# Kernel optimization log

Measured on AMD Instinct MI355X. Metric: run time of the kernel, lower is better.

Reference implementation:

```python
import jax, jax.numpy as jnp
import numpy as np
from jax import lax

K = 3
PAD = 1


def conv2d(x, w, b, pad):
    out = lax.conv_general_dilated(x, w, (1, 1), [(pad, pad), (pad, pad)],
                                   dimension_numbers=('NCHW', 'OIHW', 'NCHW'))
    return out + b[None, :, None, None]


def bilinear_sample(img, y, x):
    # img [B,C,H,W]; y,x [B,K2,H,W] float coords; zero padding outside
    H, W = img.shape[2], img.shape[3]
    y0 = jnp.floor(y)
    x0 = jnp.floor(x)
    wy = y - y0
    wx = x - x0

    def corner(yc, xc, wgt):
        valid = (yc >= 0) & (yc <= H - 1) & (xc >= 0) & (xc <= W - 1)
        yi = jnp.clip(yc, 0, H - 1).astype(jnp.int32)
        xi = jnp.clip(xc, 0, W - 1).astype(jnp.int32)
        vals = jax.vmap(lambda im, a, b_: im[:, a, b_])(img, yi, xi)  # [B,C,K2,H,W]
        return vals * (wgt * valid)[:, None]

    return (corner(y0, x0, (1 - wy) * (1 - wx)) + corner(y0, x0 + 1, (1 - wy) * wx)
            + corner(y0 + 1, x0, wy * (1 - wx)) + corner(y0 + 1, x0 + 1, wy * wx))


def dcn_v2(x, off_w, off_b, w, b):
    # ModulatedDeformConvPack: conv_offset -> (o1,o2,mask); deformable 3x3 conv, stride 1, pad 1
    B, C, H, W = x.shape
    off = conv2d(x, off_w, off_b, PAD)                      # [B,27,H,W]
    o1, o2, m = jnp.split(off, 3, axis=1)
    offset = jnp.concatenate([o1, o2], axis=1)              # [B,18,H,W]
    dy = offset[:, 0::2]                                    # [B,9,H,W]
    dx = offset[:, 1::2]
    mask = jax.nn.sigmoid(m)                                # [B,9,H,W]
    ki, kj = jnp.meshgrid(jnp.arange(K), jnp.arange(K), indexing='ij')
    ki = ki.reshape(K * K).astype(x.dtype)
    kj = kj.reshape(K * K).astype(x.dtype)
    # base sampling grid: p_y = h - pad + ki, p_x = w - pad + kj
    py = (jnp.arange(H, dtype=x.dtype)[None, :] - PAD + ki[:, None])  # [9,H]
    px = (jnp.arange(W, dtype=x.dtype)[None, :] - PAD + kj[:, None])  # [9,W]
    ys = py[None, :, :, None] + dy                           # [B,9,H,W]
    xs = px[None, :, None, :] + dx
    sampled = bilinear_sample(x, ys, xs)                     # [B,C,9,H,W]
    sampled = sampled * mask[:, None]
    out = jnp.einsum('bckhw,ock->bohw', sampled, w.reshape(w.shape[0], w.shape[1], K * K))
    return out + b[None, :, None, None]


def upsample2x(x):
    B, C, H, W = x.shape
    return jax.image.resize(x, (B, C, 2 * H, 2 * W), method='bilinear')


def forward(x, ow1, ob1, w1, b1, ow2, ob2, w2, b2, rw, rb):
    h = jax.nn.elu(dcn_v2(x, ow1, ob1, w1, b1))
    h = upsample2x(h)
    h = jax.nn.elu(dcn_v2(h, ow2, ob2, w2, b2))
    res = upsample2x(conv2d(x, rw, rb, 0))
    return h + res


def setup_inputs() -> dict:
    key = jax.random.key(0)
    ks = jax.random.split(key, 12)
    Cin, Cout = 64, 64
    B, H, W = 2, 192, 192
    f = jnp.float32
    return {
        'x': jax.random.normal(ks[0], (B, Cin, H, W), dtype=f),
        'ow1': jax.random.normal(ks[1], (27, Cin, 3, 3), dtype=f) * 0.01,
        'ob1': jax.random.normal(ks[2], (27,), dtype=f) * 0.01,
        'w1': jax.random.normal(ks[3], (Cout, Cin, 3, 3), dtype=f) * (1.0 / np.sqrt(Cin * 9)),
        'b1': jnp.zeros((Cout,), dtype=f),
        'ow2': jax.random.normal(ks[4], (27, Cout, 3, 3), dtype=f) * 0.01,
        'ob2': jax.random.normal(ks[5], (27,), dtype=f) * 0.01,
        'w2': jax.random.normal(ks[6], (Cout, Cout, 3, 3), dtype=f) * (1.0 / np.sqrt(Cout * 9)),
        'b2': jnp.zeros((Cout,), dtype=f),
        'rw': jax.random.normal(ks[7], (Cout, Cin, 1, 1), dtype=f) * (1.0 / np.sqrt(Cin)),
        'rb': jnp.zeros((Cout,), dtype=f),
    }


def reference(x, ow1, ob1, w1, b1, ow2, ob2, w2, b2, rw, rb):
    return forward(x, ow1, ob1, w1, b1, ow2, ob2, w2, b2, rw, rb)
```

## Files before the change

kernel.cpp:

```cpp
#include <hip/hip_runtime.h>
#include <math.h>

typedef unsigned short u16;
typedef __attribute__((ext_vector_type(8))) short bf16x8;
typedef __attribute__((ext_vector_type(4))) float f32x4;
typedef __attribute__((ext_vector_type(4))) unsigned u32x4;

__device__ __forceinline__ u16 f2b(float f) {
    union { float f; unsigned u; } v; v.f = f;
    unsigned r = (v.u + 0x7FFF + ((v.u >> 16) & 1)) >> 16;
    return (u16)r;
}
__device__ __forceinline__ unsigned pack2(float a, float b) {
    return (unsigned)f2b(a) | ((unsigned)f2b(b) << 16);
}
__device__ __forceinline__ void bpair(unsigned u, float& lo, float& hi) {
    union { unsigned q; float f; } a, b;
    a.q = u << 16; b.q = u & 0xFFFF0000u;
    lo = a.f; hi = b.f;
}

__global__ void prep_frag(const float* __restrict__ src, u16* __restrict__ dst,
                          int G, int KCB, int NOC, int TS) {
    int idx = blockIdx.x * 256 + threadIdx.x;
    if (idx >= KCB * G * 512) return;
    int j = idx & 7, lane = (idx >> 3) & 63, rest = idx >> 9;
    int g = rest % G, kcb = rest / G;
    int oc = g * 16 + (lane & 15);
    int c = (kcb & 1) * 32 + (lane >> 4) * 8 + j;
    int k = kcb >> 1;
    float v = (oc < NOC) ? src[((size_t)oc * 64 + c) * TS + k] : 0.f;
    dst[idx] = f2b(v);
}

template<int H, int W>
__global__ __launch_bounds__(256) void nchw2nhwc_bf16(const float* __restrict__ src,
                                                      u16* __restrict__ dst) {
    const int SEG = W / 64, HW = H * W;
    int blk = blockIdx.x;
    int b = blk / (H * SEG);
    int r = blk - b * (H * SEG);
    int h = r / SEG;
    int x0 = (r - h * SEG) * 64;
    int t = threadIdx.x;
    __shared__ float lds[64][65];
    const float* sb = src + (size_t)b * 64 * HW + (size_t)h * W + x0;
    int px = t & 63, cg = t >> 6;
#pragma unroll
    for (int i = 0; i < 16; ++i) {
        int c = cg * 16 + i;
        lds[c][px] = sb[(size_t)c * HW + px];
    }
    __syncthreads();
    u16* db = dst + ((size_t)b * HW + (size_t)h * W + x0) * 64;
    int c = t & 63, pg = t >> 6;
#pragma unroll
    for (int i = 0; i < 16; ++i) {
        int p = pg * 16 + i;
        db[(size_t)p * 64 + c] = f2b(lds[c][p]);
    }
}

__global__ __launch_bounds__(256) void upsample_nhwc_bf16(const float* __restrict__ src,
                                                          u16* __restrict__ dst) {
    const int Hh = 192, Wh = 192, H = 384, W = 384;
    int ox0 = blockIdx.x * 32;
    int oy  = blockIdx.y;
    int b   = blockIdx.z;
    int t = threadIdx.x;
    int iy  = oy >> 1;
    int oy2 = (oy & 1) ? min(iy + 1, Hh - 1) : max(iy - 1, 0);
    int ix0m1 = ox0 / 2 - 1;
    __shared__ float lds[2][64][19];
    const float* sb = src + (size_t)b * 64 * Hh * Wh;
    for (int idx = t; idx < 2 * 64 * 18; idx += 256) {
        int r2 = idx / (64 * 18);
        int rem = idx - r2 * (64 * 18);
        int c = rem / 18;
        int p = rem - c * 18;
        int gx = min(max(ix0m1 + p, 0), Wh - 1);
        int gy = r2 ? oy2 : iy;
        lds[r2][c][p] = sb[((size_t)c * Hh + gy) * Wh + gx];
    }
    __syncthreads();
    int c = t & 63, j = t >> 6;
    u16* db = dst + ((size_t)b * H * W + (size_t)oy * W + ox0) * 64;
#pragma unroll
    for (int ii = 0; ii < 8; ++ii) {
        int opx = j * 8 + ii;
        int ox = ox0 + opx;
        int ix = ox >> 1;
        int oxn = (ox & 1) ? min(ix + 1, Wh - 1) : max(ix - 1, 0);
        int il = ix - ix0m1;
        int ol = oxn - ix0m1;
        float cc = lds[0][c][il], cn = lds[0][c][ol];
        float nc = lds[1][c][il], nn = lds[1][c][ol];
        db[(size_t)opx * 64 + c] = f2b(0.5625f * cc + 0.1875f * (cn + nc) + 0.0625f * nn);
    }
}

template<int H, int W>
__global__ __launch_bounds__(256, 4) void conv_off_rA(
    const u16*  __restrict__ srcT,
    const u16*  __restrict__ wf,
    const float* __restrict__ bias,
    float* __restrict__ dst)
{
    const int HW = H * W, SEGS = W / 16;
    int t = threadIdx.x;
    int wv = t >> 6, lane = t & 63, m16 = t & 15, quad = (t >> 4) & 3;
    int seg = blockIdx.x * 4 + wv;
    int b = seg / (H * SEGS);
    int r = seg - b * (H * SEGS);
    int h = r / SEGS;
    int x0 = (r - h * SEGS) * 16;

    const u16* sb = srcT + (size_t)b * HW * 64;
    float bz0 = bias[m16];
    float bz1 = (m16 < 11) ? bias[16 + m16] : 0.f;
    f32x4 acc[2] = {{bz0,bz0,bz0,bz0},{bz1,bz1,bz1,bz1}};

#pragma unroll
    for (int k = 0; k < 9; ++k) {
        const int ki = k / 3, kj = k % 3;
        int yy = h - 1 + ki;
        int xx = x0 + m16 - 1 + kj;
        bool ok = (yy >= 0 && yy < H && xx >= 0 && xx < W);
        int yc = min(max(yy, 0), H - 1);
        int xc = min(max(xx, 0), W - 1);
        const u16* base = sb + (size_t)(yc * W + xc) * 64 + quad * 8;
#pragma unroll
        for (int cb = 0; cb < 2; ++cb) {
            u32x4 raw = *(const u32x4*)(base + cb * 32);
            union { unsigned u[4]; bf16x8 v; } A;
#pragma unroll
            for (int q = 0; q < 4; ++q) A.u[q] = ok ? raw[q] : 0u;
            const u16* wrow = wf + (size_t)((k * 2 + cb) * 2) * 512 + lane * 8;
#pragma unroll
            for (int g = 0; g < 2; ++g) {
                bf16x8 bv = *(const bf16x8*)(wrow + g * 512);
                acc[g] = __builtin_amdgcn_mfma_f32_16x16x32_bf16(A.v, bv, acc[g], 0, 0, 0);
            }
        }
    }

    int xs = x0 + quad * 4;
    float* dbase = dst + (size_t)b * 27 * HW + (size_t)h * W + xs;
    *(f32x4*)(dbase + (size_t)m16 * HW) = acc[0];
    if (m16 < 11) *(f32x4*)(dbase + (size_t)(16 + m16) * HW) = acc[1];
}

__global__ __launch_bounds__(256) void conv1x1_rA(
    const u16*  __restrict__ srcT,
    const u16*  __restrict__ wf,
    const float* __restrict__ rb,
    float* __restrict__ resT)
{
    const int H = 192, W = 192, HW = H * W, SEGS = W / 16;
    int t = threadIdx.x;
    int wv = t >> 6, lane = t & 63, m16 = t & 15, quad = (t >> 4) & 3;
    int seg = blockIdx.x * 4 + wv;
    int b = seg / (H * SEGS);
    int r = seg - b * (H * SEGS);
    int h = r / SEGS;
    int x0 = (r - h * SEGS) * 16;

    const u16* base = srcT + ((size_t)b * HW + (size_t)h * W + x0 + m16) * 64 + quad * 8;
    f32x4 acc[4];
#pragma unroll
    for (int g = 0; g < 4; ++g) { float bz = rb[g * 16 + m16]; acc[g] = {bz,bz,bz,bz}; }

#pragma unroll
    for (int cb = 0; cb < 2; ++cb) {
        bf16x8 A = *(const bf16x8*)(base + cb * 32);
        const u16* wrow = wf + (size_t)(cb * 4) * 512 + lane * 8;
#pragma unroll
        for (int g = 0; g < 4; ++g) {
            bf16x8 bv = *(const bf16x8*)(wrow + g * 512);
            acc[g] = __builtin_amdgcn_mfma_f32_16x16x32_bf16(A, bv, acc[g], 0, 0, 0);
        }
    }

    int xs = x0 + quad * 4;
    float* ob = resT + ((size_t)b * HW + (size_t)h * W) * 64;
#pragma unroll
    for (int g = 0; g < 4; ++g) {
        int oc = g * 16 + m16;
#pragma unroll
        for (int rg = 0; rg < 4; ++rg)
            ob[(size_t)(xs + rg) * 64 + oc] = acc[g][rg];
    }
}

template<int H, int W, bool ADD_RES>
__global__ __launch_bounds__(256, 4) void dcn_rA(
    const u16*  __restrict__ srcT,
    const float* __restrict__ off,
    const u16*  __restrict__ wf,
    const float* __restrict__ bias,
    const float* __restrict__ resT,
    float* __restrict__ dst)
{
    const int HW = H * W, SEGS = W / 16;
    int t = threadIdx.x;
    int wv = t >> 6, lane = t & 63, m16 = t & 15, quad = (t >> 4) & 3;
    int seg = blockIdx.x * 4 + wv;
    int b = seg / (H * SEGS);
    int r = seg - b * (H * SEGS);
    int h = r / SEGS;
    int x0 = (r - h * SEGS) * 16;

    const u16* sb = srcT + (size_t)b * HW * 64;
    const float* offp = off + (size_t)b * 27 * HW + (size_t)h * W + x0 + m16;

    float dyv[9], dxv[9], msv[9];
#pragma unroll
    for (int k = 0; k < 9; ++k) {
        dyv[k] = offp[(size_t)(2 * k) * HW];
        dxv[k] = offp[(size_t)(2 * k + 1) * HW];
        msv[k] = offp[(size_t)(18 + k) * HW];
    }

    f32x4 acc[4];
#pragma unroll
    for (int g = 0; g < 4; ++g) { float bz = bias[g * 16 + m16]; acc[g] = {bz,bz,bz,bz}; }

#pragma unroll
    for (int k = 0; k < 9; ++k) {
        const int ki = k / 3, kj = k % 3;
        float mm = 1.f / (1.f + __expf(-msv[k]));
        float yf = (float)(h - 1 + ki) + dyv[k];
        float xf = (float)(x0 + m16 - 1 + kj) + dxv[k];
        float y0f = floorf(yf), x0f = floorf(xf);
        float wy = yf - y0f, wx = xf - x0f;
        int yi = (int)y0f, xi = (int)x0f;
        float vy0 = (yi >= 0 && yi < H) ? 1.f : 0.f;
        float vy1 = (yi + 1 >= 0 && yi + 1 < H) ? 1.f : 0.f;
        float vx0 = (xi >= 0 && xi < W) ? 1.f : 0.f;
        float vx1 = (xi + 1 >= 0 && xi + 1 < W) ? 1.f : 0.f;
        float w00 = (1.f - wy) * (1.f - wx) * vy0 * vx0 * mm;
        float w01 = (1.f - wy) * wx * vy0 * vx1 * mm;
        float w10 = wy * (1.f - wx) * vy1 * vx0 * mm;
        float w11 = wy * wx * vy1 * vx1 * mm;
        int y0c = min(max(yi, 0), H - 1), y1c = min(max(yi + 1, 0), H - 1);
        int x0c = min(max(xi, 0), W - 1), x1c = min(max(xi + 1, 0), W - 1);
        const u16* p00 = sb + (size_t)(y0c * W + x0c) * 64 + quad * 8;
        const u16* p01 = sb + (size_t)(y0c * W + x1c) * 64 + quad * 8;
        const u16* p10 = sb + (size_t)(y1c * W + x0c) * 64 + quad * 8;
        const u16* p11 = sb + (size_t)(y1c * W + x1c) * 64 + quad * 8;

#pragma unroll
        for (int cb = 0; cb < 2; ++cb) {
            u32x4 r00 = *(const u32x4*)(p00 + cb * 32);
            u32x4 r01 = *(const u32x4*)(p01 + cb * 32);
            u32x4 r10 = *(const u32x4*)(p10 + cb * 32);
            u32x4 r11 = *(const u32x4*)(p11 + cb * 32);
            union { unsigned u[4]; bf16x8 v; } A;
#pragma unroll
            for (int q = 0; q < 4; ++q) {
                float a0, a1, b0, b1, c0, c1, d0, d1;
                bpair(r00[q], a0, a1); bpair(r01[q], b0, b1);
                bpair(r10[q], c0, c1); bpair(r11[q], d0, d1);
                float e = fmaf(a0, w00, fmaf(b0, w01, fmaf(c0, w10, d0 * w11)));
                float o = fmaf(a1, w00, fmaf(b1, w01, fmaf(c1, w10, d1 * w11)));
                A.u[q] = pack2(e, o);
            }
            const u16* wrow = wf + (size_t)((k * 2 + cb) * 4) * 512 + lane * 8;
#pragma unroll
            for (int g = 0; g < 4; ++g) {
                bf16x8 bv = *(const bf16x8*)(wrow + g * 512);
                acc[g] = __builtin_amdgcn_mfma_f32_16x16x32_bf16(A.v, bv, acc[g], 0, 0, 0);
            }
        }
    }

    int xs = x0 + quad * 4;
    float* dbase = dst + (size_t)b * 64 * HW + (size_t)h * W + xs;
    const int Hh = H / 2, Wh = W / 2;
    int iy = h >> 1;
    int oyn = (h & 1) ? min(iy + 1, Hh - 1) : max(iy - 1, 0);
    const float* rb0 = ADD_RES ? resT + ((size_t)b * Hh * Wh + (size_t)iy * Wh) * 64 : nullptr;
    const float* rb1 = ADD_RES ? resT + ((size_t)b * Hh * Wh + (size_t)oyn * Wh) * 64 : nullptr;
#pragma unroll
    for (int g = 0; g < 4; ++g) {
        int oc = g * 16 + m16;
        f32x4 v = acc[g];
#pragma unroll
        for (int rg = 0; rg < 4; ++rg) {
            float val = v[rg];
            val = val > 0.f ? val : (expf(val) - 1.f);
            if (ADD_RES) {
                int xq = xs + rg;
                int ix = xq >> 1;
                int oxn = (xq & 1) ? min(ix + 1, Wh - 1) : max(ix - 1, 0);
                val += 0.5625f * rb0[(size_t)ix * 64 + oc]
                     + 0.1875f * (rb0[(size_t)oxn * 64 + oc] + rb1[(size_t)ix * 64 + oc])
                     + 0.0625f * rb1[(size_t)oxn * 64 + oc];
            }
            v[rg] = val;
        }
        *(f32x4*)(dbase + (size_t)oc * HW) = v;
    }
}

extern "C" void kernel_launch(void* const* d_in, const int* in_sizes, int n_in,
                              void* d_out, int out_size, void* d_ws, size_t ws_size,
                              hipStream_t stream) {
    const float* x   = (const float*)d_in[0];
    const float* ow1 = (const float*)d_in[1];
    const float* ob1 = (const float*)d_in[2];
    const float* w1  = (const float*)d_in[3];
    const float* b1  = (const float*)d_in[4];
    const float* ow2 = (const float*)d_in[5];
    const float* ob2 = (const float*)d_in[6];
    const float* w2  = (const float*)d_in[7];
    const float* b2  = (const float*)d_in[8];
    const float* rw  = (const float*)d_in[9];
    const float* rbv = (const float*)d_in[10];
    float* out = (float*)d_out;

    float* ws   = (float*)d_ws;
    float* off1 = ws;
    float* h1   = off1 + 1990656;
    float* r    = h1   + 4718592;
    float* off2 = r    + 4718592;
    u16* xbh    = (u16*)(off2 + 7962624);
    u16* u      = xbh + 4718592;
    u16* wfd1   = u + 18874368;
    u16* wfd2   = wfd1 + 36864;
    u16* wfo1   = wfd2 + 36864;
    u16* wfo2   = wfo1 + 18432;
    u16* wf11   = wfo2 + 18432;

    prep_frag<<<144, 256, 0, stream>>>(w1,  wfd1, 4, 18, 64, 9);
    prep_frag<<<144, 256, 0, stream>>>(w2,  wfd2, 4, 18, 64, 9);
    prep_frag<<< 72, 256, 0, stream>>>(ow1, wfo1, 2, 18, 27, 9);
    prep_frag<<< 72, 256, 0, stream>>>(ow2, wfo2, 2, 18, 27, 9);
    prep_frag<<< 16, 256, 0, stream>>>(rw,  wf11, 4,  2, 64, 1);

    nchw2nhwc_bf16<192, 192><<<2 * 192 * 3, 256, 0, stream>>>(x, xbh);
    conv_off_rA<192, 192><<<(2 * 192 * 12) / 4, 256, 0, stream>>>(xbh, wfo1, ob1, off1);
    conv1x1_rA<<<(2 * 192 * 12) / 4, 256, 0, stream>>>(xbh, wf11, rbv, r);
    dcn_rA<192, 192, false><<<(2 * 192 * 12) / 4, 256, 0, stream>>>(xbh, off1, wfd1, b1, nullptr, h1);
    upsample_nhwc_bf16<<<dim3(12, 384, 2), 256, 0, stream>>>(h1, u);
    conv_off_rA<384, 384><<<(2 * 384 * 24) / 4, 256, 0, stream>>>(u, wfo2, ob2, off2);
    dcn_rA<384, 384, true><<<(2 * 384 * 24) / 4, 256, 0, stream>>>(u, off2, wfd2, b2, r, out);
}
```

Before: 461.8 us.

## Prefetch offsets, hoist corner loads, pack bilinear FMAs, and precompute residual in LDS

The deformable conv kernel now software-pipelines the offset/mask loads one kernel tap ahead and issues all eight corner gathers for a tap before the weight math. This is meant to hide global-memory latency and cut register pressure from the 27 preloaded offsets. Bilinear blending uses packed 2-wide FMAs and the hardware v_cvt_pk_bf16_f32 instruction in place of manual rounding. The upsampled residual is computed cooperatively into shared memory with coalesced per-lane channel reads, replacing strided scattered reads in the epilogue. This costs extra LDS and a different rounding path for the bf16 conversion.

```diff
diff --git a/kernel.cpp b/kernel.cpp
--- a/kernel.cpp
+++ b/kernel.cpp
@@ -4,20 +4,29 @@
 typedef unsigned short u16;
 typedef __attribute__((ext_vector_type(8))) short bf16x8;
 typedef __attribute__((ext_vector_type(4))) float f32x4;
+typedef __attribute__((ext_vector_type(2))) float f32x2;
 typedef __attribute__((ext_vector_type(4))) unsigned u32x4;
+typedef __attribute__((ext_vector_type(2))) unsigned u32x2;
 
 __device__ __forceinline__ u16 f2b(float f) {
     union { float f; unsigned u; } v; v.f = f;
     unsigned r = (v.u + 0x7FFF + ((v.u >> 16) & 1)) >> 16;
     return (u16)r;
 }
-__device__ __forceinline__ unsigned pack2(float a, float b) {
-    return (unsigned)f2b(a) | ((unsigned)f2b(b) << 16);
-}
-__device__ __forceinline__ void bpair(unsigned u, float& lo, float& hi) {
-    union { unsigned q; float f; } a, b;
-    a.q = u << 16; b.q = u & 0xFFFF0000u;
-    lo = a.f; hi = b.f;
+
+__device__ __forceinline__ f32x2 unpk(unsigned u) {
+    union { u32x2 q; f32x2 f; } v;
+    v.q.x = u << 16;
+    v.q.y = u & 0xFFFF0000u;
+    return v.f;
+}
+__device__ __forceinline__ unsigned cvt_pk(f32x2 e) {
+    unsigned r;
+    asm("v_cvt_pk_bf16_f32 %0, %1, %2" : "=v"(r) : "v"(e.x), "v"(e.y));
+    return r;
+}
+__device__ __forceinline__ f32x2 pkfma(f32x2 a, f32x2 b, f32x2 c) {
+    return __builtin_elementwise_fma(a, b, c);
 }
 
 __global__ void prep_frag(const float* __restrict__ src, u16* __restrict__ dst,
@@ -213,12 +222,32 @@
     const u16* sb = srcT + (size_t)b * HW * 64;
     const float* offp = off + (size_t)b * 27 * HW + (size_t)h * W + x0 + m16;
 
-    float dyv[9], dxv[9], msv[9];
-#pragma unroll
-    for (int k = 0; k < 9; ++k) {
-        dyv[k] = offp[(size_t)(2 * k) * HW];
-        dxv[k] = offp[(size_t)(2 * k + 1) * HW];
-        msv[k] = offp[(size_t)(18 + k) * HW];
+    __shared__ float lres[4][16][65];
+
+    float dyc = offp[0];
+    float dxc = offp[(size_t)HW];
+    float msc = offp[(size_t)18 * HW];
+
+    if (ADD_RES) {
+        const int Hh = H / 2, Wh = W / 2;
+        int iy = h >> 1;
+        int oyn = (h & 1) ? min(iy + 1, Hh - 1) : max(iy - 1, 0);
+        const float* r0row = resT + ((size_t)b * Hh * Wh + (size_t)iy  * Wh) * 64 + lane;
+        const float* r1row = resT + ((size_t)b * Hh * Wh + (size_t)oyn * Wh) * 64 + lane;
+        int ixb = x0 >> 1;
+        float a0 = r0row[(size_t)max(ixb - 1, 0) * 64];
+        float a1 = r1row[(size_t)max(ixb - 1, 0) * 64];
+        float b0 = r0row[(size_t)ixb * 64];
+        float b1 = r1row[(size_t)ixb * 64];
+#pragma unroll
+        for (int m = 0; m < 8; ++m) {
+            int ixn = min(ixb + m + 1, Wh - 1);
+            float c0 = r0row[(size_t)ixn * 64];
+            float c1 = r1row[(size_t)ixn * 64];
+            lres[wv][2 * m][lane]     = 0.5625f * b0 + 0.1875f * (a0 + b1) + 0.0625f * a1;
+            lres[wv][2 * m + 1][lane] = 0.5625f * b0 + 0.1875f * (c0 + b1) + 0.0625f * c1;
+            a0 = b0; a1 = b1; b0 = c0; b1 = c1;
+        }
     }
 
     f32x4 acc[4];
@@ -228,12 +257,31 @@
 #pragma unroll
     for (int k = 0; k < 9; ++k) {
         const int ki = k / 3, kj = k % 3;
-        float mm = 1.f / (1.f + __expf(-msv[k]));
-        float yf = (float)(h - 1 + ki) + dyv[k];
-        float xf = (float)(x0 + m16 - 1 + kj) + dxv[k];
+        float dyn_ = 0.f, dxn_ = 0.f, msn_ = 0.f;
+        if (k < 8) {
+            dyn_ = offp[(size_t)(2 * k + 2) * HW];
+            dxn_ = offp[(size_t)(2 * k + 3) * HW];
+            msn_ = offp[(size_t)(19 + k) * HW];
+        }
+
+        float yf = (float)(h - 1 + ki) + dyc;
+        float xf = (float)(x0 + m16 - 1 + kj) + dxc;
         float y0f = floorf(yf), x0f = floorf(xf);
+        int yi = (int)y0f, xi = (int)x0f;
+        int y0c = min(max(yi, 0), H - 1), y1c = min(max(yi + 1, 0), H - 1);
+        int x0c = min(max(xi, 0), W - 1), x1c = min(max(xi + 1, 0), W - 1);
+        const u16* p00 = sb + (size_t)(y0c * W + x0c) * 64 + quad * 8;
+        const u16* p01 = sb + (size_t)(y0c * W + x1c) * 64 + quad * 8;
+        const u16* p10 = sb + (size_t)(y1c * W + x0c) * 64 + quad * 8;
+        const u16* p11 = sb + (size_t)(y1c * W + x1c) * 64 + quad * 8;
+
+        u32x4 r00a = *(const u32x4*)p00,        r00b = *(const u32x4*)(p00 + 32);
+        u32x4 r01a = *(const u32x4*)p01,        r01b = *(const u32x4*)(p01 + 32);
+        u32x4 r10a = *(const u32x4*)p10,        r10b = *(const u32x4*)(p10 + 32);
+        u32x4 r11a = *(const u32x4*)p11,        r11b = *(const u32x4*)(p11 + 32);
+
+        float mm = 1.f / (1.f + __expf(-msc));
         float wy = yf - y0f, wx = xf - x0f;
-        int yi = (int)y0f, xi = (int)x0f;
         float vy0 = (yi >= 0 && yi < H) ? 1.f : 0.f;
         float vy1 = (yi + 1 >= 0 && yi + 1 < H) ? 1.f : 0.f;
         float vx0 = (xi >= 0 && xi < W) ? 1.f : 0.f;
@@ -242,28 +290,18 @@
         float w01 = (1.f - wy) * wx * vy0 * vx1 * mm;
         float w10 = wy * (1.f - wx) * vy1 * vx0 * mm;
         float w11 = wy * wx * vy1 * vx1 * mm;
-        int y0c = min(max(yi, 0), H - 1), y1c = min(max(yi + 1, 0), H - 1);
-        int x0c = min(max(xi, 0), W - 1), x1c = min(max(xi + 1, 0), W - 1);
-        const u16* p00 = sb + (size_t)(y0c * W + x0c) * 64 + quad * 8;
-        const u16* p01 = sb + (size_t)(y0c * W + x1c) * 64 + quad * 8;
-        const u16* p10 = sb + (size_t)(y1c * W + x0c) * 64 + quad * 8;
-        const u16* p11 = sb + (size_t)(y1c * W + x1c) * 64 + quad * 8;
+        f32x2 W00 = {w00, w00}, W01 = {w01, w01}, W10 = {w10, w10}, W11 = {w11, w11};
 
 #pragma unroll
         for (int cb = 0; cb < 2; ++cb) {
-            u32x4 r00 = *(const u32x4*)(p00 + cb * 32);
-            u32x4 r01 = *(const u32x4*)(p01 + cb * 32);
-            u32x4 r10 = *(const u32x4*)(p10 + cb * 32);
-            u32x4 r11 = *(const u32x4*)(p11 + cb * 32);
             union { unsigned u[4]; bf16x8 v; } A;
 #pragma unroll
             for (int q = 0; q < 4; ++q) {
-                float a0, a1, b0, b1, c0, c1, d0, d1;
-                bpair(r00[q], a0, a1); bpair(r01[q], b0, b1);
-                bpair(r10[q], c0, c1); bpair(r11[q], d0, d1);
-                float e = fmaf(a0, w00, fmaf(b0, w01, fmaf(c0, w10, d0 * w11)));
-                float o = fmaf(a1, w00, fmaf(b1, w01, fmaf(c1, w10, d1 * w11)));
-                A.u[q] = pack2(e, o);
+                f32x2 s = pkfma(unpk(cb ? r01b[q] : r01a[q]), W01,
+                                unpk(cb ? r00b[q] : r00a[q]) * W00);
+                s = pkfma(unpk(cb ? r10b[q] : r10a[q]), W10, s);
+                s = pkfma(unpk(cb ? r11b[q] : r11a[q]), W11, s);
+                A.u[q] = cvt_pk(s);
             }
             const u16* wrow = wf + (size_t)((k * 2 + cb) * 4) * 512 + lane * 8;
 #pragma unroll
@@ -272,15 +310,12 @@
                 acc[g] = __builtin_amdgcn_mfma_f32_16x16x32_bf16(A.v, bv, acc[g], 0, 0, 0);
             }
         }
+
+        if (k < 8) { dyc = dyn_; dxc = dxn_; msc = msn_; }
     }
 
     int xs = x0 + quad * 4;
     float* dbase = dst + (size_t)b * 64 * HW + (size_t)h * W + xs;
-    const int Hh = H / 2, Wh = W / 2;
-    int iy = h >> 1;
-    int oyn = (h & 1) ? min(iy + 1, Hh - 1) : max(iy - 1, 0);
-    const float* rb0 = ADD_RES ? resT + ((size_t)b * Hh * Wh + (size_t)iy * Wh) * 64 : nullptr;
-    const float* rb1 = ADD_RES ? resT + ((size_t)b * Hh * Wh + (size_t)oyn * Wh) * 64 : nullptr;
 #pragma unroll
     for (int g = 0; g < 4; ++g) {
         int oc = g * 16 + m16;
@@ -289,14 +324,7 @@
         for (int rg = 0; rg < 4; ++rg) {
             float val = v[rg];
             val = val > 0.f ? val : (expf(val) - 1.f);
-            if (ADD_RES) {
-                int xq = xs + rg;
-                int ix = xq >> 1;
-                int oxn = (xq & 1) ? min(ix + 1, Wh - 1) : max(ix - 1, 0);
-                val += 0.5625f * rb0[(size_t)ix * 64 + oc]
-                     + 0.1875f * (rb0[(size_t)oxn * 64 + oc] + rb1[(size_t)ix * 64 + oc])
-                     + 0.0625f * rb1[(size_t)oxn * 64 + oc];
-            }
+            if (ADD_RES) val += lres[wv][quad * 4 + rg][oc];
             v[rg] = val;
         }
         *(f32x4*)(dbase + (size_t)oc * HW) = v;
```

After: 459.7 us. No clear change (-0.5%).
